# Optimization experiments

Hardware: AMD Instinct MI355X
Metric: run time of the kernel (lower is better)

## Reference

```python
import jax, jax.numpy as jnp
import numpy as np

DELTA_V = 0.5
DELTA_D = 1.5
ALPHA = 1.0
BETA = 1.0
GAMMA = 0.001
K = 33  # segment count: id 0 = background, 1..32 = instances (matches fill_max)


def setup_inputs() -> dict:
    key = jax.random.key(0)
    k1, k2 = jax.random.split(key)
    embeddings = jax.random.normal(k1, (8, 16, 512, 512), dtype=jnp.float32)
    instance_masks = jax.random.randint(k2, (8, 512, 512), 0, K, dtype=jnp.int32)
    return {"embeddings": embeddings, "instance_masks": instance_masks}


def _safe_norm(sq):
    # sqrt with zero-safe gradient: returns 0 where sq == 0
    pos = sq > 0
    return jnp.sqrt(jnp.where(pos, sq, 1.0)) * pos.astype(sq.dtype)


def _per_image(emb, mask):
    # emb: (E, H, W), mask: (H, W)
    E = emb.shape[0]
    emb_flat = emb.reshape(E, -1).T            # (N, E)
    ids = mask.reshape(-1)                      # (N,)

    counts = jax.ops.segment_sum(jnp.ones(ids.shape, jnp.float32), ids, num_segments=K)  # (K,)
    sums = jax.ops.segment_sum(emb_flat, ids, num_segments=K)                             # (K, E)
    counts_c = jnp.maximum(counts, 1.0)
    means = sums / counts_c[:, None]            # (K, E)

    present = counts[1:] > 0                    # (K-1,) which instance ids appear
    n_inst = present.sum().astype(jnp.float32)

    # variance (pull) term: per-pixel distance to own instance mean
    diff = emb_flat - means[ids]                # (N, E)
    pix_d = _safe_norm(jnp.sum(diff * diff, axis=1))
    var_term = jnp.maximum(pix_d - DELTA_V, 0.0) ** 2
    var_per = jax.ops.segment_sum(var_term, ids, num_segments=K)[1:]  # drop background seg
    var_loss = jnp.sum(jnp.where(present, var_per / counts_c[1:], 0.0)) / jnp.maximum(n_inst, 1.0)

    # distance (push) term: pairwise centroid distances among present instances
    m = means[1:]                               # (K-1, E)
    dsq = jnp.sum((m[:, None, :] - m[None, :, :]) ** 2, axis=-1)
    dmat = _safe_norm(dsq)
    pair_mask = (jnp.triu(jnp.ones((K - 1, K - 1), bool), 1)
                 & present[:, None] & present[None, :])
    n_pairs = pair_mask.sum().astype(jnp.float32)
    dist_term = jnp.maximum(2.0 * DELTA_D - dmat, 0.0) ** 2
    dist_loss = jnp.sum(jnp.where(pair_mask, dist_term, 0.0)) / jnp.maximum(n_pairs, 1.0)
    dist_loss = dist_loss * (n_inst > 1.0).astype(jnp.float32)

    # regularization: mean centroid norm over present instances
    mean_norms = _safe_norm(jnp.sum(m * m, axis=1))
    reg_loss = jnp.sum(jnp.where(present, mean_norms, 0.0)) / jnp.maximum(n_inst, 1.0)

    valid = (n_inst > 0.0).astype(jnp.float32)
    return var_loss * valid, dist_loss * valid, reg_loss * valid, valid


def reference(embeddings, instance_masks):
    v, d, r, valid = jax.vmap(_per_image)(embeddings, instance_masks)
    vs = jnp.maximum(valid.sum(), 1.0)
    var_loss = v.sum() / vs
    dist_loss = d.sum() / vs
    reg_loss = r.sum() / vs
    total = ALPHA * var_loss + BETA * dist_loss + GAMMA * reg_loss
    return jnp.stack([total, var_loss, dist_loss, reg_loss])
```

## Files before the change

### kernel.cpp

```cpp
#include <hip/hip_runtime.h>
#include <math.h>


#define B 8
#define E 16
#define HW (512*512)
#define BLK 256
#define P1_BPI 128
#define P2_BPI 128
#define P2_VPB (HW / 4 / P2_BPI)

typedef __attribute__((ext_vector_type(8)))  short short8;
typedef __attribute__((ext_vector_type(16))) float floatx16;

__device__ __forceinline__ float atomAddF(float* p, float v) {
  return unsafeAtomicAdd(p, v);
}

__device__ __forceinline__ unsigned pack_bf(float a, float b) {
  return __builtin_amdgcn_perm(__float_as_uint(b), __float_as_uint(a), 0x07060302u);
}

__global__ __launch_bounds__(BLK) void pass1_kernel(
    const float* __restrict__ emb, const int* __restrict__ mask,
    float* __restrict__ gsum ) {
  __shared__ int4 mstage[4][128];
  __shared__ __align__(16) float lred[4][32][33];
  const int b    = blockIdx.y;
  const int t    = threadIdx.x;
  const int lane = t & 63;
  const int wv   = __builtin_amdgcn_readfirstlane(t >> 6);
  const int n    = lane & 31;
  const int h    = lane >> 5;
  const int myid = n + 1;
  const bool ld  = (n < 16);

  const int ppw    = HW / (P1_BPI * 4);
  const int ntiles = ppw / 16;
  const int base   = (blockIdx.x * 4 + wv) * ppw;

  {
    const int4* __restrict__ mg = (const int4*)(mask + (size_t)b * HW + base);
    mstage[wv][lane]      = mg[lane];
    mstage[wv][64 + lane] = mg[64 + lane];
  }
  __syncthreads();

  const float* __restrict__ pl = emb + ((size_t)b * E + (n & 15)) * HW + base + 8 * h;

  floatx16 acc;
#pragma unroll
  for (int i = 0; i < 16; ++i) acc[i] = 0.f;

  float4 fb[4][2];
#pragma unroll
  for (int u = 0; u < 4; ++u) {
    if (ld) {
      fb[u][0] = ((const float4*)(pl + u * 16))[0];
      fb[u][1] = ((const float4*)(pl + u * 16))[1];
    }
  }

  for (int tl4 = 0; tl4 < ntiles; tl4 += 4) {
#pragma unroll
    for (int u = 0; u < 4; ++u) {
      const int tl = tl4 + u;

      const int4 A0 = mstage[wv][tl * 4 + 2 * h];
      const int4 A1 = mstage[wv][tl * 4 + 2 * h + 1];

      short8 af;
      af[0] = (A0.x == myid) ? (short)0x3F80 : (short)0;
      af[1] = (A0.y == myid) ? (short)0x3F80 : (short)0;
      af[2] = (A0.z == myid) ? (short)0x3F80 : (short)0;
      af[3] = (A0.w == myid) ? (short)0x3F80 : (short)0;
      af[4] = (A1.x == myid) ? (short)0x3F80 : (short)0;
      af[5] = (A1.y == myid) ? (short)0x3F80 : (short)0;
      af[6] = (A1.z == myid) ? (short)0x3F80 : (short)0;
      af[7] = (A1.w == myid) ? (short)0x3F80 : (short)0;

      short8 bf;
      if (ld) {
        union { uint4 u4; short8 s; } cv;
        cv.u4.x = pack_bf(fb[u][0].x, fb[u][0].y);
        cv.u4.y = pack_bf(fb[u][0].z, fb[u][0].w);
        cv.u4.z = pack_bf(fb[u][1].x, fb[u][1].y);
        cv.u4.w = pack_bf(fb[u][1].z, fb[u][1].w);
        bf = cv.s;
      } else if (n == 16) {
        const short one = (short)0x3F80;
        bf[0]=one; bf[1]=one; bf[2]=one; bf[3]=one; bf[4]=one; bf[5]=one; bf[6]=one; bf[7]=one;
      } else {
        bf[0]=0; bf[1]=0; bf[2]=0; bf[3]=0; bf[4]=0; bf[5]=0; bf[6]=0; bf[7]=0;
      }

      acc = __builtin_amdgcn_mfma_f32_32x32x16_bf16(af, bf, acc, 0, 0, 0);

      const int tn = tl + 4;
      if (tn < ntiles && ld) {
        fb[u][0] = ((const float4*)(pl + tn * 16))[0];
        fb[u][1] = ((const float4*)(pl + tn * 16))[1];
      }
    }
  }

#pragma unroll
  for (int r = 0; r < 16; ++r) {
    const int row = (r & 3) + 8 * (r >> 2) + 4 * h;
    lred[wv][row][n] = acc[r];
  }
  __syncthreads();

  for (int i = t; i < 32 * 32; i += BLK) {
    const int row = i >> 5, col = i & 31;
    if (col < 17) {
      const float s = lred[0][row][col] + lred[1][row][col]
                    + lred[2][row][col] + lred[3][row][col];
      atomAddF(&gsum[((size_t)b * 32 + row) * 17 + col], s);
    }
  }
}

__global__ __launch_bounds__(BLK) void pass2_kernel(
    const float* __restrict__ emb, const int* __restrict__ mask,
    const float* __restrict__ gsum, float* __restrict__ vsum ) {
  __shared__ __align__(16) float mean4[33][4][4];
  __shared__ float winv[33];
  __shared__ float wred[4];
  const int b = blockIdx.y;
  const int t = threadIdx.x;

  for (int i = t; i < 33 * 16; i += BLK) {
    const int k = i >> 4, e = i & 15;
    float m = 0.f;
    if (k >= 1) {
      const float cnt = gsum[((size_t)b * 32 + (k - 1)) * 17 + 16];
      const float cc  = cnt > 1.f ? cnt : 1.f;
      m = gsum[((size_t)b * 32 + (k - 1)) * 17 + e] / cc;
    }
    const int j = e >> 2;
    mean4[k][(j + k + (k >> 2)) & 3][e & 3] = m;
  }
  if (t < 33) {
    float w = 0.f;
    if (t >= 1) {
      const float cnt = gsum[((size_t)b * 32 + (t - 1)) * 17 + 16];
      w = cnt > 0.5f ? 1.f / cnt : 0.f;
    }
    winv[t] = w;
  }
  __syncthreads();

  const int4*  __restrict__ maskv = (const int4*)(mask + (size_t)b * HW);
  const float* __restrict__ embb  = emb + (size_t)b * E * HW;
  const int v0 = blockIdx.x * P2_VPB;
  float vacc = 0.f;

#pragma unroll 1
  for (int v = v0 + t; v < v0 + P2_VPB; v += BLK) {
    const int4 id = maskv[v];
    float4 x[E];
#pragma unroll
    for (int e = 0; e < E; ++e) x[e] = ((const float4*)(embb + (size_t)e * HW))[v];

    const int sx = id.x + (id.x >> 2);
    const int sy = id.y + (id.y >> 2);
    const int sz = id.z + (id.z >> 2);
    const int sw = id.w + (id.w >> 2);

    float d0 = 0.f, d1 = 0.f, d2 = 0.f, d3 = 0.f;
#pragma unroll
    for (int j = 0; j < 4; ++j) {
      const float4 m0 = *(const float4*)&mean4[id.x][(j + sx) & 3][0];
      const float4 m1 = *(const float4*)&mean4[id.y][(j + sy) & 3][0];
      const float4 m2 = *(const float4*)&mean4[id.z][(j + sz) & 3][0];
      const float4 m3 = *(const float4*)&mean4[id.w][(j + sw) & 3][0];
      const float4 a0 = x[4 * j + 0], a1 = x[4 * j + 1];
      const float4 a2 = x[4 * j + 2], a3 = x[4 * j + 3];
      float u;
      u = a0.x - m0.x; d0 += u * u;  u = a1.x - m0.y; d0 += u * u;
      u = a2.x - m0.z; d0 += u * u;  u = a3.x - m0.w; d0 += u * u;
      u = a0.y - m1.x; d1 += u * u;  u = a1.y - m1.y; d1 += u * u;
      u = a2.y - m1.z; d1 += u * u;  u = a3.y - m1.w; d1 += u * u;
      u = a0.z - m2.x; d2 += u * u;  u = a1.z - m2.y; d2 += u * u;
      u = a2.z - m2.z; d2 += u * u;  u = a3.z - m2.w; d2 += u * u;
      u = a0.w - m3.x; d3 += u * u;  u = a1.w - m3.y; d3 += u * u;
      u = a2.w - m3.z; d3 += u * u;  u = a3.w - m3.w; d3 += u * u;
    }
    float hh;
    hh = fmaxf(sqrtf(d0) - 0.5f, 0.f); vacc += hh * hh * winv[id.x];
    hh = fmaxf(sqrtf(d1) - 0.5f, 0.f); vacc += hh * hh * winv[id.y];
    hh = fmaxf(sqrtf(d2) - 0.5f, 0.f); vacc += hh * hh * winv[id.z];
    hh = fmaxf(sqrtf(d3) - 0.5f, 0.f); vacc += hh * hh * winv[id.w];
  }

#pragma unroll
  for (int off = 32; off >= 1; off >>= 1) vacc += __shfl_down(vacc, off, 64);
  if ((t & 63) == 0) wred[t >> 6] = vacc;
  __syncthreads();
  if (t == 0) atomAddF(&vsum[b], wred[0] + wred[1] + wred[2] + wred[3]);
}

__global__ __launch_bounds__(BLK) void final_kernel(
    const float* __restrict__ gsum, const float* __restrict__ vsum,
    float* __restrict__ out) {
  __shared__ float mean[B][32][E];
  __shared__ float cnts[B][32];
  __shared__ float rb[B], db[B], pb[B], nb[B];
  const int t = threadIdx.x;

  if (t < B) { rb[t] = 0.f; db[t] = 0.f; pb[t] = 0.f; nb[t] = 0.f; }
  {
    const int bb = t >> 5, k = t & 31;
    const float c  = gsum[((size_t)bb * 32 + k) * 17 + 16];
    const float cc = c > 1.f ? c : 1.f;
    cnts[bb][k] = c;
#pragma unroll
    for (int e = 0; e < E; ++e)
      mean[bb][k][e] = gsum[((size_t)bb * 32 + k) * 17 + e] / cc;
  }
  __syncthreads();

  {
    const int bb = t >> 5, k = t & 31;
    const float c = cnts[bb][k];
    if (c > 0.5f) {
      atomAddF(&nb[bb], 1.f);
      float sq = 0.f;
#pragma unroll
      for (int e = 0; e < E; ++e) { const float m = mean[bb][k][e]; sq += m * m; }
      atomAddF(&rb[bb], sq > 0.f ? sqrtf(sq) : 0.f);
    }
  }
  __syncthreads();

  for (int idx = t; idx < B * 32 * 32; idx += BLK) {
    const int bb = idx >> 10;
    const int p  = idx & 1023;
    const int i  = p >> 5;
    const int j  = p & 31;
    if (i < j && cnts[bb][i] > 0.5f && cnts[bb][j] > 0.5f) {
      atomAddF(&pb[bb], 1.f);
      float sq = 0.f;
#pragma unroll
      for (int e = 0; e < E; ++e) {
        const float d = mean[bb][i][e] - mean[bb][j][e];
        sq += d * d;
      }
      const float dn = sq > 0.f ? sqrtf(sq) : 0.f;
      const float hh = 3.0f - dn;
      if (hh > 0.f) atomAddF(&db[bb], hh * hh);
    }
  }
  __syncthreads();

  if (t == 0) {
    float sv = 0.f, sd = 0.f, sr = 0.f, svalid = 0.f;
    for (int bb = 0; bb < B; ++bb) {
      const float ni  = nb[bb];
      const float nim = ni > 1.f ? ni : 1.f;
      const float var_b = vsum[bb] / nim;
      const float reg_b = rb[bb] / nim;
      const float npm   = pb[bb] > 1.f ? pb[bb] : 1.f;
      const float dist_b = (ni > 1.f) ? (db[bb] / npm) : 0.f;
      const float valid  = ni > 0.f ? 1.f : 0.f;
      sv += var_b * valid;
      sd += dist_b * valid;
      sr += reg_b * valid;
      svalid += valid;
    }
    const float vs = svalid > 1.f ? svalid : 1.f;
    const float var = sv / vs, dist = sd / vs, reg = sr / vs;
    out[0] = var + dist + 0.001f * reg;
    out[1] = var;
    out[2] = dist;
    out[3] = reg;
  }
}

extern "C" void kernel_launch(void* const* d_in, const int* in_sizes, int n_in,
                              void* d_out, int out_size, void* d_ws, size_t ws_size,
                              hipStream_t stream) {
  const float* emb  = (const float*)d_in[0];
  const int*   mask = (const int*)d_in[1];
  float* out = (float*)d_out;

  float* gsum = (float*)d_ws;
  float* vsum = (float*)((char*)d_ws + (size_t)B * 32 * 17 * 4);

  hipMemsetAsync(d_ws, 0, (size_t)(B * 32 * 17 + B) * 4, stream);

  pass1_kernel<<<dim3(P1_BPI, B), BLK, 0, stream>>>(emb, mask, gsum);
  pass2_kernel<<<dim3(P2_BPI, B), BLK, 0, stream>>>(emb, mask, gsum, vsum);
  final_kernel<<<1, BLK, 0, stream>>>(gsum, vsum, out);
}
```

Baseline: 250.4 us.

## Fuse three passes into one persistent kernel with per-image flag barriers

New measurement: 645.2 us. +157.6%, slower.

```diff
diff --git a/kernel.cpp b/kernel.cpp
--- a/kernel.cpp
+++ b/kernel.cpp
@@ -6,9 +6,11 @@
 #define E 16
 #define HW (512*512)
 #define BLK 256
-#define P1_BPI 128
-#define P2_BPI 128
-#define P2_VPB (HW / 4 / P2_BPI)
+#define P_BPI 128
+#define GRID (P_BPI * B)
+#define PPW 512
+#define NTILES (PPW / 16)
+#define P2_VPB 512
 
 typedef __attribute__((ext_vector_type(8)))  short short8;
 typedef __attribute__((ext_vector_type(16))) float floatx16;
@@ -21,214 +23,233 @@
   return __builtin_amdgcn_perm(__float_as_uint(b), __float_as_uint(a), 0x07060302u);
 }
 
-__global__ __launch_bounds__(BLK) void pass1_kernel(
+union Smem {
+  struct { int4 mstage[4][128]; float lred[4][32][33]; } p1;
+  struct { float mean4[33][4][4]; float winv[33]; } p2;
+  struct { float mean[B][32][E]; float cnts[B][32]; } fin;
+};
+
+__global__ __launch_bounds__(BLK, 4) void fused_kernel(
     const float* __restrict__ emb, const int* __restrict__ mask,
-    float* __restrict__ gsum ) {
-  __shared__ int4 mstage[4][128];
-  __shared__ __align__(16) float lred[4][32][33];
-  const int b    = blockIdx.y;
-  const int t    = threadIdx.x;
-  const int lane = t & 63;
-  const int wv   = __builtin_amdgcn_readfirstlane(t >> 6);
-  const int n    = lane & 31;
-  const int h    = lane >> 5;
-  const int myid = n + 1;
-  const bool ld  = (n < 16);
-
-  const int ppw    = HW / (P1_BPI * 4);
-  const int ntiles = ppw / 16;
-  const int base   = (blockIdx.x * 4 + wv) * ppw;
+    float* __restrict__ gsum , float* __restrict__ vsum ,
+    int* __restrict__ flags , int* __restrict__ done ,
+    float* __restrict__ out) {
+  __shared__ Smem sm;
+  __shared__ float wred[4];
+  __shared__ float rb[B], db[B], pb[B], nb[B];
+  __shared__ int lastblk;
+
+  const int blk   = blockIdx.x;
+  const int b     = blk >> 7;
+  const int slice = blk & 127;
+  const int t     = threadIdx.x;
+  const int lane  = t & 63;
+  const int wv    = __builtin_amdgcn_readfirstlane(t >> 6);
 
   {
-    const int4* __restrict__ mg = (const int4*)(mask + (size_t)b * HW + base);
-    mstage[wv][lane]      = mg[lane];
-    mstage[wv][64 + lane] = mg[64 + lane];
-  }
-  __syncthreads();
-
-  const float* __restrict__ pl = emb + ((size_t)b * E + (n & 15)) * HW + base + 8 * h;
-
-  floatx16 acc;
-#pragma unroll
-  for (int i = 0; i < 16; ++i) acc[i] = 0.f;
-
-  float4 fb[4][2];
-#pragma unroll
-  for (int u = 0; u < 4; ++u) {
-    if (ld) {
-      fb[u][0] = ((const float4*)(pl + u * 16))[0];
-      fb[u][1] = ((const float4*)(pl + u * 16))[1];
-    }
-  }
-
-  for (int tl4 = 0; tl4 < ntiles; tl4 += 4) {
+    const int n    = lane & 31;
+    const int h    = lane >> 5;
+    const int myid = n + 1;
+    const bool ld  = (n < 16);
+    const int wbase = (slice * 4 + wv) * PPW;
+
+    {
+      const int4* __restrict__ mg = (const int4*)(mask + (size_t)b * HW + wbase);
+      sm.p1.mstage[wv][lane]      = mg[lane];
+      sm.p1.mstage[wv][64 + lane] = mg[64 + lane];
+    }
+    __syncthreads();
+
+    const float* __restrict__ pl = emb + ((size_t)b * E + (n & 15)) * HW + wbase + 8 * h;
+
+    floatx16 acc;
+#pragma unroll
+    for (int i = 0; i < 16; ++i) acc[i] = 0.f;
+
+    float4 fb[4][2];
 #pragma unroll
     for (int u = 0; u < 4; ++u) {
-      const int tl = tl4 + u;
-
-      const int4 A0 = mstage[wv][tl * 4 + 2 * h];
-      const int4 A1 = mstage[wv][tl * 4 + 2 * h + 1];
-
-      short8 af;
-      af[0] = (A0.x == myid) ? (short)0x3F80 : (short)0;
-      af[1] = (A0.y == myid) ? (short)0x3F80 : (short)0;
-      af[2] = (A0.z == myid) ? (short)0x3F80 : (short)0;
-      af[3] = (A0.w == myid) ? (short)0x3F80 : (short)0;
-      af[4] = (A1.x == myid) ? (short)0x3F80 : (short)0;
-      af[5] = (A1.y == myid) ? (short)0x3F80 : (short)0;
-      af[6] = (A1.z == myid) ? (short)0x3F80 : (short)0;
-      af[7] = (A1.w == myid) ? (short)0x3F80 : (short)0;
-
-      short8 bf;
       if (ld) {
-        union { uint4 u4; short8 s; } cv;
-        cv.u4.x = pack_bf(fb[u][0].x, fb[u][0].y);
-        cv.u4.y = pack_bf(fb[u][0].z, fb[u][0].w);
-        cv.u4.z = pack_bf(fb[u][1].x, fb[u][1].y);
-        cv.u4.w = pack_bf(fb[u][1].z, fb[u][1].w);
-        bf = cv.s;
-      } else if (n == 16) {
-        const short one = (short)0x3F80;
-        bf[0]=one; bf[1]=one; bf[2]=one; bf[3]=one; bf[4]=one; bf[5]=one; bf[6]=one; bf[7]=one;
-      } else {
-        bf[0]=0; bf[1]=0; bf[2]=0; bf[3]=0; bf[4]=0; bf[5]=0; bf[6]=0; bf[7]=0;
-      }
-
-      acc = __builtin_amdgcn_mfma_f32_32x32x16_bf16(af, bf, acc, 0, 0, 0);
-
-      const int tn = tl + 4;
-      if (tn < ntiles && ld) {
-        fb[u][0] = ((const float4*)(pl + tn * 16))[0];
-        fb[u][1] = ((const float4*)(pl + tn * 16))[1];
-      }
-    }
-  }
-
-#pragma unroll
-  for (int r = 0; r < 16; ++r) {
-    const int row = (r & 3) + 8 * (r >> 2) + 4 * h;
-    lred[wv][row][n] = acc[r];
-  }
-  __syncthreads();
-
-  for (int i = t; i < 32 * 32; i += BLK) {
-    const int row = i >> 5, col = i & 31;
-    if (col < 17) {
-      const float s = lred[0][row][col] + lred[1][row][col]
-                    + lred[2][row][col] + lred[3][row][col];
-      atomAddF(&gsum[((size_t)b * 32 + row) * 17 + col], s);
-    }
-  }
-}
-
-__global__ __launch_bounds__(BLK) void pass2_kernel(
-    const float* __restrict__ emb, const int* __restrict__ mask,
-    const float* __restrict__ gsum, float* __restrict__ vsum ) {
-  __shared__ __align__(16) float mean4[33][4][4];
-  __shared__ float winv[33];
-  __shared__ float wred[4];
-  const int b = blockIdx.y;
-  const int t = threadIdx.x;
-
-  for (int i = t; i < 33 * 16; i += BLK) {
-    const int k = i >> 4, e = i & 15;
-    float m = 0.f;
-    if (k >= 1) {
-      const float cnt = gsum[((size_t)b * 32 + (k - 1)) * 17 + 16];
-      const float cc  = cnt > 1.f ? cnt : 1.f;
-      m = gsum[((size_t)b * 32 + (k - 1)) * 17 + e] / cc;
-    }
-    const int j = e >> 2;
-    mean4[k][(j + k + (k >> 2)) & 3][e & 3] = m;
-  }
-  if (t < 33) {
-    float w = 0.f;
-    if (t >= 1) {
-      const float cnt = gsum[((size_t)b * 32 + (t - 1)) * 17 + 16];
-      w = cnt > 0.5f ? 1.f / cnt : 0.f;
-    }
-    winv[t] = w;
-  }
-  __syncthreads();
-
-  const int4*  __restrict__ maskv = (const int4*)(mask + (size_t)b * HW);
-  const float* __restrict__ embb  = emb + (size_t)b * E * HW;
-  const int v0 = blockIdx.x * P2_VPB;
-  float vacc = 0.f;
+        fb[u][0] = ((const float4*)(pl + u * 16))[0];
+        fb[u][1] = ((const float4*)(pl + u * 16))[1];
+      }
+    }
+
+    for (int tl4 = 0; tl4 < NTILES; tl4 += 4) {
+#pragma unroll
+      for (int u = 0; u < 4; ++u) {
+        const int tl = tl4 + u;
+        const int4 A0 = sm.p1.mstage[wv][tl * 4 + 2 * h];
+        const int4 A1 = sm.p1.mstage[wv][tl * 4 + 2 * h + 1];
+
+        short8 af;
+        af[0] = (A0.x == myid) ? (short)0x3F80 : (short)0;
+        af[1] = (A0.y == myid) ? (short)0x3F80 : (short)0;
+        af[2] = (A0.z == myid) ? (short)0x3F80 : (short)0;
+        af[3] = (A0.w == myid) ? (short)0x3F80 : (short)0;
+        af[4] = (A1.x == myid) ? (short)0x3F80 : (short)0;
+        af[5] = (A1.y == myid) ? (short)0x3F80 : (short)0;
+        af[6] = (A1.z == myid) ? (short)0x3F80 : (short)0;
+        af[7] = (A1.w == myid) ? (short)0x3F80 : (short)0;
+
+        short8 bf;
+        if (ld) {
+          union { uint4 u4; short8 s; } cv;
+          cv.u4.x = pack_bf(fb[u][0].x, fb[u][0].y);
+          cv.u4.y = pack_bf(fb[u][0].z, fb[u][0].w);
+          cv.u4.z = pack_bf(fb[u][1].x, fb[u][1].y);
+          cv.u4.w = pack_bf(fb[u][1].z, fb[u][1].w);
+          bf = cv.s;
+        } else if (n == 16) {
+          const short one = (short)0x3F80;
+          bf[0]=one; bf[1]=one; bf[2]=one; bf[3]=one; bf[4]=one; bf[5]=one; bf[6]=one; bf[7]=one;
+        } else {
+          bf[0]=0; bf[1]=0; bf[2]=0; bf[3]=0; bf[4]=0; bf[5]=0; bf[6]=0; bf[7]=0;
+        }
+
+        acc = __builtin_amdgcn_mfma_f32_32x32x16_bf16(af, bf, acc, 0, 0, 0);
+
+        const int tn = tl + 4;
+        if (tn < NTILES && ld) {
+          fb[u][0] = ((const float4*)(pl + tn * 16))[0];
+          fb[u][1] = ((const float4*)(pl + tn * 16))[1];
+        }
+      }
+    }
+
+#pragma unroll
+    for (int r = 0; r < 16; ++r) {
+      const int row = (r & 3) + 8 * (r >> 2) + 4 * h;
+      sm.p1.lred[wv][row][n] = acc[r];
+    }
+    __syncthreads();
+
+    for (int i = t; i < 32 * 32; i += BLK) {
+      const int row = i >> 5, col = i & 31;
+      if (col < 17) {
+        const float s = sm.p1.lred[0][row][col] + sm.p1.lred[1][row][col]
+                      + sm.p1.lred[2][row][col] + sm.p1.lred[3][row][col];
+        atomAddF(&gsum[((size_t)b * 32 + row) * 17 + col], s);
+      }
+    }
+  }
+
+  __threadfence();
+  __syncthreads();
+  if (t == 0)
+    __hip_atomic_fetch_add(&flags[b], 1, __ATOMIC_RELEASE, __HIP_MEMORY_SCOPE_AGENT);
+
+  if (t == 0) {
+    long it = 0;
+    while (__hip_atomic_load(&flags[b], __ATOMIC_ACQUIRE, __HIP_MEMORY_SCOPE_AGENT) < P_BPI) {
+      __builtin_amdgcn_s_sleep(8);
+      if (++it > 200000000L) break;
+    }
+  }
+  __syncthreads();
+  __threadfence();
+
+  {
+    for (int i = t; i < 33 * 16; i += BLK) {
+      const int k = i >> 4, e = i & 15;
+      float m = 0.f;
+      if (k >= 1) {
+        const float cnt = gsum[((size_t)b * 32 + (k - 1)) * 17 + 16];
+        const float cc  = cnt > 1.f ? cnt : 1.f;
+        m = gsum[((size_t)b * 32 + (k - 1)) * 17 + e] / cc;
+      }
+      const int j = e >> 2;
+      sm.p2.mean4[k][(j + k + (k >> 2)) & 3][e & 3] = m;
+    }
+    if (t < 33) {
+      float w = 0.f;
+      if (t >= 1) {
+        const float cnt = gsum[((size_t)b * 32 + (t - 1)) * 17 + 16];
+        w = cnt > 0.5f ? 1.f / cnt : 0.f;
+      }
+      sm.p2.winv[t] = w;
+    }
+    __syncthreads();
+
+    const int4*  __restrict__ maskv = (const int4*)(mask + (size_t)b * HW);
+    const float* __restrict__ embb  = emb + (size_t)b * E * HW;
+    const int v0 = slice * P2_VPB;
+    float vacc = 0.f;
 
 #pragma unroll 1
-  for (int v = v0 + t; v < v0 + P2_VPB; v += BLK) {
-    const int4 id = maskv[v];
-    float4 x[E];
-#pragma unroll
-    for (int e = 0; e < E; ++e) x[e] = ((const float4*)(embb + (size_t)e * HW))[v];
-
-    const int sx = id.x + (id.x >> 2);
-    const int sy = id.y + (id.y >> 2);
-    const int sz = id.z + (id.z >> 2);
-    const int sw = id.w + (id.w >> 2);
-
-    float d0 = 0.f, d1 = 0.f, d2 = 0.f, d3 = 0.f;
-#pragma unroll
-    for (int j = 0; j < 4; ++j) {
-      const float4 m0 = *(const float4*)&mean4[id.x][(j + sx) & 3][0];
-      const float4 m1 = *(const float4*)&mean4[id.y][(j + sy) & 3][0];
-      const float4 m2 = *(const float4*)&mean4[id.z][(j + sz) & 3][0];
-      const float4 m3 = *(const float4*)&mean4[id.w][(j + sw) & 3][0];
-      const float4 a0 = x[4 * j + 0], a1 = x[4 * j + 1];
-      const float4 a2 = x[4 * j + 2], a3 = x[4 * j + 3];
-      float u;
-      u = a0.x - m0.x; d0 += u * u;  u = a1.x - m0.y; d0 += u * u;
-      u = a2.x - m0.z; d0 += u * u;  u = a3.x - m0.w; d0 += u * u;
-      u = a0.y - m1.x; d1 += u * u;  u = a1.y - m1.y; d1 += u * u;
-      u = a2.y - m1.z; d1 += u * u;  u = a3.y - m1.w; d1 += u * u;
-      u = a0.z - m2.x; d2 += u * u;  u = a1.z - m2.y; d2 += u * u;
-      u = a2.z - m2.z; d2 += u * u;  u = a3.z - m2.w; d2 += u * u;
-      u = a0.w - m3.x; d3 += u * u;  u = a1.w - m3.y; d3 += u * u;
-      u = a2.w - m3.z; d3 += u * u;  u = a3.w - m3.w; d3 += u * u;
-    }
-    float hh;
-    hh = fmaxf(sqrtf(d0) - 0.5f, 0.f); vacc += hh * hh * winv[id.x];
-    hh = fmaxf(sqrtf(d1) - 0.5f, 0.f); vacc += hh * hh * winv[id.y];
-    hh = fmaxf(sqrtf(d2) - 0.5f, 0.f); vacc += hh * hh * winv[id.z];
-    hh = fmaxf(sqrtf(d3) - 0.5f, 0.f); vacc += hh * hh * winv[id.w];
-  }
-
-#pragma unroll
-  for (int off = 32; off >= 1; off >>= 1) vacc += __shfl_down(vacc, off, 64);
-  if ((t & 63) == 0) wred[t >> 6] = vacc;
-  __syncthreads();
-  if (t == 0) atomAddF(&vsum[b], wred[0] + wred[1] + wred[2] + wred[3]);
-}
-
-__global__ __launch_bounds__(BLK) void final_kernel(
-    const float* __restrict__ gsum, const float* __restrict__ vsum,
-    float* __restrict__ out) {
-  __shared__ float mean[B][32][E];
-  __shared__ float cnts[B][32];
-  __shared__ float rb[B], db[B], pb[B], nb[B];
-  const int t = threadIdx.x;
+    for (int v = v0 + t; v < v0 + P2_VPB; v += BLK) {
+      const int4 id = maskv[v];
+      float4 x[E];
+#pragma unroll
+      for (int e = 0; e < E; ++e) x[e] = ((const float4*)(embb + (size_t)e * HW))[v];
+
+      const int sx = id.x + (id.x >> 2);
+      const int sy = id.y + (id.y >> 2);
+      const int sz = id.z + (id.z >> 2);
+      const int sw = id.w + (id.w >> 2);
+
+      float d0 = 0.f, d1 = 0.f, d2 = 0.f, d3 = 0.f;
+#pragma unroll
+      for (int j = 0; j < 4; ++j) {
+        const float4 m0 = *(const float4*)&sm.p2.mean4[id.x][(j + sx) & 3][0];
+        const float4 m1 = *(const float4*)&sm.p2.mean4[id.y][(j + sy) & 3][0];
+        const float4 m2 = *(const float4*)&sm.p2.mean4[id.z][(j + sz) & 3][0];
+        const float4 m3 = *(const float4*)&sm.p2.mean4[id.w][(j + sw) & 3][0];
+        const float4 a0 = x[4 * j + 0], a1 = x[4 * j + 1];
+        const float4 a2 = x[4 * j + 2], a3 = x[4 * j + 3];
+        float u;
+        u = a0.x - m0.x; d0 += u * u;  u = a1.x - m0.y; d0 += u * u;
+        u = a2.x - m0.z; d0 += u * u;  u = a3.x - m0.w; d0 += u * u;
+        u = a0.y - m1.x; d1 += u * u;  u = a1.y - m1.y; d1 += u * u;
+        u = a2.y - m1.z; d1 += u * u;  u = a3.y - m1.w; d1 += u * u;
+        u = a0.z - m2.x; d2 += u * u;  u = a1.z - m2.y; d2 += u * u;
+        u = a2.z - m2.z; d2 += u * u;  u = a3.z - m2.w; d2 += u * u;
+        u = a0.w - m3.x; d3 += u * u;  u = a1.w - m3.y; d3 += u * u;
+        u = a2.w - m3.z; d3 += u * u;  u = a3.w - m3.w; d3 += u * u;
+      }
+      float hh;
+      hh = fmaxf(sqrtf(d0) - 0.5f, 0.f); vacc += hh * hh * sm.p2.winv[id.x];
+      hh = fmaxf(sqrtf(d1) - 0.5f, 0.f); vacc += hh * hh * sm.p2.winv[id.y];
+      hh = fmaxf(sqrtf(d2) - 0.5f, 0.f); vacc += hh * hh * sm.p2.winv[id.z];
+      hh = fmaxf(sqrtf(d3) - 0.5f, 0.f); vacc += hh * hh * sm.p2.winv[id.w];
+    }
+
+#pragma unroll
+    for (int off = 32; off >= 1; off >>= 1) vacc += __shfl_down(vacc, off, 64);
+    if ((t & 63) == 0) wred[t >> 6] = vacc;
+    __syncthreads();
+    if (t == 0) atomAddF(&vsum[b], wred[0] + wred[1] + wred[2] + wred[3]);
+  }
+
+  if (t == 0) {
+    __threadfence();
+    const int old = __hip_atomic_fetch_add(done, 1, __ATOMIC_ACQ_REL, __HIP_MEMORY_SCOPE_AGENT);
+    lastblk = (old == GRID - 1) ? 1 : 0;
+  }
+  __syncthreads();
+  if (!lastblk) return;
+  __threadfence();
 
   if (t < B) { rb[t] = 0.f; db[t] = 0.f; pb[t] = 0.f; nb[t] = 0.f; }
   {
     const int bb = t >> 5, k = t & 31;
     const float c  = gsum[((size_t)bb * 32 + k) * 17 + 16];
     const float cc = c > 1.f ? c : 1.f;
-    cnts[bb][k] = c;
+    sm.fin.cnts[bb][k] = c;
 #pragma unroll
     for (int e = 0; e < E; ++e)
-      mean[bb][k][e] = gsum[((size_t)bb * 32 + k) * 17 + e] / cc;
+      sm.fin.mean[bb][k][e] = gsum[((size_t)bb * 32 + k) * 17 + e] / cc;
   }
   __syncthreads();
 
   {
     const int bb = t >> 5, k = t & 31;
-    const float c = cnts[bb][k];
+    const float c = sm.fin.cnts[bb][k];
     if (c > 0.5f) {
       atomAddF(&nb[bb], 1.f);
       float sq = 0.f;
 #pragma unroll
-      for (int e = 0; e < E; ++e) { const float m = mean[bb][k][e]; sq += m * m; }
+      for (int e = 0; e < E; ++e) { const float m = sm.fin.mean[bb][k][e]; sq += m * m; }
       atomAddF(&rb[bb], sq > 0.f ? sqrtf(sq) : 0.f);
     }
   }
@@ -239,12 +260,12 @@
     const int p  = idx & 1023;
     const int i  = p >> 5;
     const int j  = p & 31;
-    if (i < j && cnts[bb][i] > 0.5f && cnts[bb][j] > 0.5f) {
+    if (i < j && sm.fin.cnts[bb][i] > 0.5f && sm.fin.cnts[bb][j] > 0.5f) {
       atomAddF(&pb[bb], 1.f);
       float sq = 0.f;
 #pragma unroll
       for (int e = 0; e < E; ++e) {
-        const float d = mean[bb][i][e] - mean[bb][j][e];
+        const float d = sm.fin.mean[bb][i][e] - sm.fin.mean[bb][j][e];
         sq += d * d;
       }
       const float dn = sq > 0.f ? sqrtf(sq) : 0.f;
@@ -285,12 +306,12 @@
   const int*   mask = (const int*)d_in[1];
   float* out = (float*)d_out;
 
-  float* gsum = (float*)d_ws;
-  float* vsum = (float*)((char*)d_ws + (size_t)B * 32 * 17 * 4);
-
-  hipMemsetAsync(d_ws, 0, (size_t)(B * 32 * 17 + B) * 4, stream);
-
-  pass1_kernel<<<dim3(P1_BPI, B), BLK, 0, stream>>>(emb, mask, gsum);
-  pass2_kernel<<<dim3(P2_BPI, B), BLK, 0, stream>>>(emb, mask, gsum, vsum);
-  final_kernel<<<1, BLK, 0, stream>>>(gsum, vsum, out);
+  float* gsum  = (float*)d_ws;
+  float* vsum  = (float*)((char*)d_ws + (size_t)(B * 32 * 17) * 4);
+  int*   flags = (int*)((char*)d_ws + (size_t)(B * 32 * 17 + B) * 4);
+  int*   done  = (int*)((char*)d_ws + (size_t)(B * 32 * 17 + 2 * B) * 4);
+
+  hipMemsetAsync(d_ws, 0, (size_t)(B * 32 * 17 + 2 * B + 1) * 4, stream);
+
+  fused_kernel<<<GRID, BLK, 0, stream>>>(emb, mask, gsum, vsum, flags, done, out);
 }
```
